# Kernel optimization log

Hardware: AMD Instinct MI355X
Metric: run time of the kernel (lower is better)

## Reference

```python
import jax, jax.numpy as jnp
import numpy as np


def setup_inputs() -> dict:
    key = jax.random.key(0)
    x = jax.random.normal(key, (32, 64, 64, 64), dtype=jnp.float32)
    return {"x": x, "num_zeros": 2}


def reference(x, num_zeros):
    # ZeroWeave: interleave `num_zeros` zeros between every pair of pixels
    # along both spatial dims (equivalent to the gather_nd over
    # concat([x, zeros_like(x)]) with the precomputed index tensor).
    # x: [B, C, H, W] -> [B, C, H*s - num_zeros, W*s - num_zeros], s = num_zeros + 1
    s = num_zeros + 1
    B, C, H, W = x.shape
    out_h = H * s - num_zeros
    out_w = W * s - num_zeros
    out = jnp.zeros((B, C, out_h, out_w), dtype=x.dtype)
    out = out.at[:, :, ::s, ::s].set(x)
    return out
```

## Files before the change

### kernel.cpp

```cpp
#include <hip/hip_runtime.h>


constexpr int PLANE_IN   = 64 * 64;
constexpr int PLANE_OUT4 = 190 * 190 / 4;
constexpr int GROUP4     = 285;
constexpr int NPLANES    = 32 * 64;
constexpr int BLOCK      = 256;
constexpr int FULL_ITERS = PLANE_OUT4 / BLOCK;
constexpr int TAIL       = PLANE_OUT4 - FULL_ITERS * BLOCK;

__global__ __launch_bounds__(BLOCK, 8) void ZeroWeave_89601607729830_kernel(
    const float* __restrict__ x, float* __restrict__ out) {
    __shared__ float    xs[PLANE_IN];
    __shared__ unsigned tab[GROUP4];

    const int bc = blockIdx.x;
    const int t  = threadIdx.x;

    {
        const float4* xp = reinterpret_cast<const float4*>(x + bc * PLANE_IN);
        float4* xl = reinterpret_cast<float4*>(xs);
#pragma unroll
        for (int k = 0; k < PLANE_IN / 4 / BLOCK; ++k)
            xl[k * BLOCK + t] = xp[k * BLOCK + t];
    }

    for (int p = t; p < GROUP4; p += BLOCK) {
        unsigned packed = 0;
#pragma unroll
        for (int j = 0; j < 4; ++j) {
            unsigned e  = 4u * p + j;
            unsigned h  = (e * 44151u) >> 23;
            unsigned w  = e - h * 190u;
            unsigned h3 = (h * 171u) >> 9;
            unsigned hm = h - h3 * 3u;
            unsigned w3 = (w * 171u) >> 9;
            unsigned wm = w - w3 * 3u;
            unsigned src = ((hm | wm) == 0u) ? (h3 * 64u + w3) : 255u;
            packed |= src << (8 * j);
        }
        tab[p] = packed;
    }
    __syncthreads();

    float4* op = reinterpret_cast<float4*>(out) + bc * PLANE_OUT4;

    auto emit = [&](int q) {
        unsigned g     = ((unsigned)q * 58868u) >> 24;
        unsigned p     = (unsigned)q - g * 285u;
        unsigned xbase = g << 7;
        unsigned packed = tab[p];
        float4 v;
        float* vp = reinterpret_cast<float*>(&v);
#pragma unroll
        for (int j = 0; j < 4; ++j) {
            unsigned b = (packed >> (8 * j)) & 255u;
            float val  = xs[(xbase + b) & (PLANE_IN - 1)];
            vp[j] = (b != 255u) ? val : 0.0f;
        }
        op[q] = v;
    };

#pragma unroll 4
    for (int k = 0; k < FULL_ITERS; ++k)
        emit(k * BLOCK + t);
    if (t < TAIL)
        emit(FULL_ITERS * BLOCK + t);
}

extern "C" void kernel_launch(void* const* d_in, const int* in_sizes, int n_in,
                              void* d_out, int out_size, void* d_ws, size_t ws_size,
                              hipStream_t stream) {
    const float* x = (const float*)d_in[0];
    float* out = (float*)d_out;

    ZeroWeave_89601607729830_kernel<<<NPLANES, BLOCK, 0, stream>>>(x, out);
}
```

Baseline: 328.4 us.

## Write zero rows directly and stream data rows from global without LDS staging

Replaces the LDS-staged, table-driven gather with a direct mapping. Each thread loads float2 pairs from global memory and writes the corresponding float4 of the data rows. Separate threads store plain zero float4s for the all-zero rows. This removes shared memory, the lookup table build, the barrier and the per-element gather arithmetic, which should raise occupancy and cut instruction overhead. In exchange, the indexing is hand-derived and fragile, and the block size changes to 192.

```diff
diff --git a/kernel.cpp b/kernel.cpp
--- a/kernel.cpp
+++ b/kernel.cpp
@@ -1,71 +1,61 @@
 #include <hip/hip_runtime.h>
 
 
-constexpr int PLANE_IN   = 64 * 64;
-constexpr int PLANE_OUT4 = 190 * 190 / 4;
-constexpr int GROUP4     = 285;
 constexpr int NPLANES    = 32 * 64;
-constexpr int BLOCK      = 256;
-constexpr int FULL_ITERS = PLANE_OUT4 / BLOCK;
-constexpr int TAIL       = PLANE_OUT4 - FULL_ITERS * BLOCK;
+constexpr int BLOCK      = 192;
+constexpr int PLANE_IN_F = 64 * 64;
+constexpr int PLANE_OUT4 = 9025;
+constexpr int GROUPS     = 31;
 
-__global__ __launch_bounds__(BLOCK, 8) void ZeroWeave_89601607729830_kernel(
+__global__ __launch_bounds__(BLOCK) void ZeroWeave_89601607729830_kernel(
     const float* __restrict__ x, float* __restrict__ out) {
-    __shared__ float    xs[PLANE_IN];
-    __shared__ unsigned tab[GROUP4];
-
     const int bc = blockIdx.x;
     const int t  = threadIdx.x;
 
+    const float* xp = x + (size_t)bc * PLANE_IN_F;
+    float4* op = reinterpret_cast<float4*>(out) + (size_t)bc * PLANE_OUT4;
+
     {
-        const float4* xp = reinterpret_cast<const float4*>(x + bc * PLANE_IN);
-        float4* xl = reinterpret_cast<float4*>(xs);
-#pragma unroll
-        for (int k = 0; k < PLANE_IN / 4 / BLOCK; ++k)
-            xl[k * BLOCK + t] = xp[k * BLOCK + t];
+        const int hi   = (t >= 96) ? 1 : 0;
+        const int r    = t - 96 * hi;
+        const int half = (r >= 48) ? 1 : 0;
+        const int rr   = r - 48 * half;
+        const unsigned c = (unsigned)rr / 3u;
+        const unsigned m = (unsigned)rr - 3u * c;
+        unsigned cls = m + (unsigned)half;
+        if (cls >= 3u) cls -= 3u;
+        const int sel2 = half ? (m == 2u) : (m != 0u);
+        const int xoff = half * 64 + 4 * (int)c + 2 * sel2;
+        const int qofs = r + (half ? 94 : 0);
+        const bool p0 = (cls == 0u), p1 = (cls == 1u), p2 = (cls == 2u);
+
+        const float* xa = xp + xoff;
+        float4* oa = op + qofs;
+#pragma unroll 4
+        for (int k = 0; k < 16; ++k) {
+            const int g = 2 * k + hi;
+            const float2 v = *reinterpret_cast<const float2*>(xa + g * 128);
+            float4 o;
+            o.x = p0 ? v.x : 0.0f;
+            o.y = p2 ? v.y : 0.0f;
+            o.z = p1 ? v.x : 0.0f;
+            o.w = p0 ? v.y : 0.0f;
+            oa[g * 285] = o;
+        }
     }
 
-    for (int p = t; p < GROUP4; p += BLOCK) {
-        unsigned packed = 0;
+    {
+        const float4 z = make_float4(0.0f, 0.0f, 0.0f, 0.0f);
+        if (t < 189) {
+            const int myq = 48 + t + ((t >= 94) ? 48 : 0);
+            float4* o = op + myq;
 #pragma unroll
-        for (int j = 0; j < 4; ++j) {
-            unsigned e  = 4u * p + j;
-            unsigned h  = (e * 44151u) >> 23;
-            unsigned w  = e - h * 190u;
-            unsigned h3 = (h * 171u) >> 9;
-            unsigned hm = h - h3 * 3u;
-            unsigned w3 = (w * 171u) >> 9;
-            unsigned wm = w - w3 * 3u;
-            unsigned src = ((hm | wm) == 0u) ? (h3 * 64u + w3) : 255u;
-            packed |= src << (8 * j);
+            for (int g = 0; g < GROUPS; ++g)
+                o[g * 285] = z;
+            if (t < 94)
+                o[GROUPS * 285] = z;
         }
-        tab[p] = packed;
     }
-    __syncthreads();
-
-    float4* op = reinterpret_cast<float4*>(out) + bc * PLANE_OUT4;
-
-    auto emit = [&](int q) {
-        unsigned g     = ((unsigned)q * 58868u) >> 24;
-        unsigned p     = (unsigned)q - g * 285u;
-        unsigned xbase = g << 7;
-        unsigned packed = tab[p];
-        float4 v;
-        float* vp = reinterpret_cast<float*>(&v);
-#pragma unroll
-        for (int j = 0; j < 4; ++j) {
-            unsigned b = (packed >> (8 * j)) & 255u;
-            float val  = xs[(xbase + b) & (PLANE_IN - 1)];
-            vp[j] = (b != 255u) ? val : 0.0f;
-        }
-        op[q] = v;
-    };
-
-#pragma unroll 4
-    for (int k = 0; k < FULL_ITERS; ++k)
-        emit(k * BLOCK + t);
-    if (t < TAIL)
-        emit(FULL_ITERS * BLOCK + t);
 }
 
 extern "C" void kernel_launch(void* const* d_in, const int* in_sizes, int n_in,
```

Result: slower. 358.7 us (+9.2%).
